# Kernel tuning notes

Measured on AMD Instinct MI355X. Metric: run time of the kernel, lower is better.

## Reference

```python
import jax, jax.numpy as jnp
import numpy as np

# Dims derived from Config for the 'ffn' pool
L, S, SE, D, K, B = 7, 200, 240, 32, 3, 512


def setup_inputs() -> dict:
    key = jax.random.key(0)
    k1, k2, k3, k4 = jax.random.split(key, 4)
    x = jax.random.normal(k1, (L, B, D), dtype=jnp.float32)
    vec_clusters = jax.random.normal(k2, (L, S, D), dtype=jnp.float32) * 0.02
    vec = jax.random.normal(k3, (L, S, SE, D), dtype=jnp.float32) * 0.02
    gain_factors = jnp.ones((L, S, SE, 2), dtype=jnp.float32)
    block_indices = jax.random.randint(k4, (L, S, SE, 2), 0, 600).astype(jnp.int32)
    return {
        'x': x,
        'vec_clusters': vec_clusters,
        'vec': vec,
        'gain_factors': gain_factors,
        'block_indices': block_indices,
    }


def reference(x, vec_clusters, vec, gain_factors, block_indices):
    # Router: score each token's query against cluster centroids. [L,B,S]
    logits = jnp.einsum('lbd,lsd->lbs', x, vec_clusters)
    top_vals, top_idx = jax.lax.top_k(logits, K)            # [L,B,K]
    probs = jax.nn.softmax(top_vals, axis=-1)               # [L,B,K]

    # Per-layer gather of the selected clusters' capacity slots.
    gather = jax.vmap(lambda tbl, idx: tbl[idx])            # map over L
    g_vec = gather(vec, top_idx)                            # [L,B,K,SE,D]
    g_gain = gather(gain_factors[..., 0], top_idx)          # [L,B,K,SE]
    g_blk = gather(block_indices[..., 0], top_idx)          # [L,B,K,SE]

    # Empty capacity slots have block index 0 (randint started at 1 in init).
    w = jax.nn.sigmoid(g_gain) * (g_blk != 0).astype(g_gain.dtype)  # [L,B,K,SE]

    # Compose parameter vectors within each selected cluster, then mix top-k.
    comp = jnp.einsum('lbke,lbked->lbkd', w, g_vec)         # [L,B,K,D]
    out = jnp.einsum('lbk,lbkd->lbd', probs, comp)          # [L,B,D]
    return out
```

## Files before the change

### kernel.cpp

```cpp
#include <hip/hip_runtime.h>
#include <math.h>

namespace {
constexpr int L = 7, S = 200, SE = 240, D = 32, B = 512;
constexpr int NTOK = L * B;
constexpr int NCLUST = L * S;
constexpr int GRID1 = NCLUST + NTOK;

template <int CTRL>
__device__ __forceinline__ float dppf(float x) {
  return __int_as_float(__builtin_amdgcn_update_dpp(
      0, __float_as_int(x), CTRL, 0xF, 0xF, true));
}
template <int CTRL>
__device__ __forceinline__ int dppi(int x) {
  return __builtin_amdgcn_update_dpp(0, x, CTRL, 0xF, 0xF, true);
}
__device__ __forceinline__ float swz16f(float x) {
  return __int_as_float(__builtin_amdgcn_ds_swizzle(__float_as_int(x), 0x401F));
}
__device__ __forceinline__ int swz16i(int x) {
  return __builtin_amdgcn_ds_swizzle(x, 0x401F);
}

__global__ __launch_bounds__(64) void fused1_kernel(
    const float* __restrict__ x,
    const float* __restrict__ vc,
    const float* __restrict__ vec,
    const float* __restrict__ gain,
    const int* __restrict__ blk,
    float* __restrict__ C,
    int4* __restrict__ tki,
    float4* __restrict__ tkp)
{
  const int lane = threadIdx.x;
  const int q = lane & 7;
  const int r8 = lane >> 3;

  if (blockIdx.x < NCLUST) {
    const int ls = blockIdx.x;
    __shared__ float sw[SE];
    for (int e = lane; e < SE; e += 64) {
      const float2 g2 = reinterpret_cast<const float2*>(gain)[ls * SE + e];
      const int2 b2 = reinterpret_cast<const int2*>(blk)[ls * SE + e];
      sw[e] = (b2.x != 0) ? 1.0f / (1.0f + __expf(-g2.x)) : 0.0f;
    }
    __syncthreads();
    const float4* v4 = reinterpret_cast<const float4*>(vec) + (size_t)ls * SE * 8;
    float4 acc = make_float4(0.f, 0.f, 0.f, 0.f);
#pragma unroll 10
    for (int k = 0; k < 30; ++k) {
      const int e = k * 8 + r8;
      const float we = sw[e];
      const float4 v = v4[e * 8 + q];
      acc.x += we * v.x; acc.y += we * v.y; acc.z += we * v.z; acc.w += we * v.w;
    }
    acc.x += dppf<0x128>(acc.x); acc.y += dppf<0x128>(acc.y);
    acc.z += dppf<0x128>(acc.z); acc.w += dppf<0x128>(acc.w);
    acc.x += swz16f(acc.x); acc.y += swz16f(acc.y);
    acc.z += swz16f(acc.z); acc.w += swz16f(acc.w);
    acc.x += __shfl_xor(acc.x, 32); acc.y += __shfl_xor(acc.y, 32);
    acc.z += __shfl_xor(acc.z, 32); acc.w += __shfl_xor(acc.w, 32);
    if (r8 == 0) reinterpret_cast<float4*>(C + ls * D)[q] = acc;
  } else {
    const int tok = blockIdx.x - NCLUST;
    const int l = tok >> 9;

    const float4 xq = reinterpret_cast<const float4*>(x + tok * D)[q];
    const float* vcl = vc + l * S * D;

    float v0 = -INFINITY, v1 = -INFINITY, v2 = -INFINITY;
    int i0 = 0x7fffffff, i1 = 0x7fffffff, i2 = 0x7fffffff;
    for (int s0 = 0; s0 < S; s0 += 8) {
      const int row = s0 + r8;
      const float4 v = reinterpret_cast<const float4*>(vcl + row * D)[q];
      float part = v.x * xq.x + v.y * xq.y + v.z * xq.z + v.w * xq.w;
      part += dppf<0xB1>(part);
      part += dppf<0x4E>(part);
      part += dppf<0x141>(part);
      if (part > v0) { v2 = v1; i2 = i1; v1 = v0; i1 = i0; v0 = part; i0 = row; }
      else if (part > v1) { v2 = v1; i2 = i1; v1 = part; i1 = row; }
      else if (part > v2) { v2 = part; i2 = row; }
    }
#pragma unroll
    for (int step = 0; step < 3; ++step) {
      float u0, u1, u2; int j0, j1, j2;
      if (step == 0) {
        u0 = dppf<0x128>(v0); u1 = dppf<0x128>(v1); u2 = dppf<0x128>(v2);
        j0 = dppi<0x128>(i0); j1 = dppi<0x128>(i1); j2 = dppi<0x128>(i2);
      } else if (step == 1) {
        u0 = swz16f(v0); u1 = swz16f(v1); u2 = swz16f(v2);
        j0 = swz16i(i0); j1 = swz16i(i1); j2 = swz16i(i2);
      } else {
        u0 = __shfl_xor(v0, 32); u1 = __shfl_xor(v1, 32); u2 = __shfl_xor(v2, 32);
        j0 = __shfl_xor(i0, 32); j1 = __shfl_xor(i1, 32); j2 = __shfl_xor(i2, 32);
      }
#pragma unroll
      for (int t = 0; t < 3; ++t) {
        const float u = (t == 0) ? u0 : (t == 1) ? u1 : u2;
        const int j = (t == 0) ? j0 : (t == 1) ? j1 : j2;
        const bool b0 = (u > v0) || (u == v0 && j < i0);
        const bool b1 = (u > v1) || (u == v1 && j < i1);
        const bool b2 = (u > v2) || (u == v2 && j < i2);
        if (b0) { v2 = v1; i2 = i1; v1 = v0; i1 = i0; v0 = u; i0 = j; }
        else if (b1) { v2 = v1; i2 = i1; v1 = u; i1 = j; }
        else if (b2) { v2 = u; i2 = j; }
      }
    }
    if (lane == 0) {
      const float e1 = __expf(v1 - v0);
      const float e2 = __expf(v2 - v0);
      const float inv = 1.f / (1.f + e1 + e2);
      tki[tok] = make_int4(i0, i1, i2, 0);
      tkp[tok] = make_float4(inv, e1 * inv, e2 * inv, 0.f);
    }
  }
}

__global__ __launch_bounds__(256) void gather_kernel(
    const float* __restrict__ C,
    const int4* __restrict__ tki,
    const float4* __restrict__ tkp,
    float* __restrict__ out)
{
  const int gid = blockIdx.x * 256 + threadIdx.x;
  const int tok = gid >> 5;
  const int d = gid & 31;
  const int l = tok >> 9;
  const int4 id = tki[tok];
  const float4 p = tkp[tok];
  const float* Cl = C + l * S * D;
  out[gid] = p.x * Cl[id.x * D + d] + p.y * Cl[id.y * D + d] + p.z * Cl[id.z * D + d];
}

}

extern "C" void kernel_launch(void* const* d_in, const int* in_sizes, int n_in,
                              void* d_out, int out_size, void* d_ws, size_t ws_size,
                              hipStream_t stream) {
  const float* x = (const float*)d_in[0];
  const float* vc = (const float*)d_in[1];
  const float* vec = (const float*)d_in[2];
  const float* gain = (const float*)d_in[3];
  const int* blk = (const int*)d_in[4];
  float* out = (float*)d_out;

  char* ws = (char*)d_ws;
  float* C = (float*)ws;
  int4* tki = (int4*)(ws + 179200);
  float4* tkp = (float4*)(ws + 179200 + 57344);

  fused1_kernel<<<GRID1, 64, 0, stream>>>(x, vc, vec, gain, blk, C, tki, tkp);
  gather_kernel<<<NTOK * D / 256, 256, 0, stream>>>(C, tki, tkp, out);
}
```

Baseline: 26.53 us.

## Make the fused router/compose kernel persistent with per-wave task loop

Replaces the launch of one 64-thread block per cluster or token with a fixed grid of 256 blocks of 8 waves. Each wave strides over a combined list of cluster-compose and token-routing tasks. Each wave gets its own shared-memory weight buffer, so the block-wide barrier is gone. This is meant to cut block scheduling overhead, but it caps residency at 8 waves per CU, which may hide memory latency less well and can leave waves unevenly loaded.

```diff
diff --git a/kernel.cpp b/kernel.cpp
--- a/kernel.cpp
+++ b/kernel.cpp
@@ -5,7 +5,10 @@
 constexpr int L = 7, S = 200, SE = 240, D = 32, B = 512;
 constexpr int NTOK = L * B;
 constexpr int NCLUST = L * S;
-constexpr int GRID1 = NCLUST + NTOK;
+constexpr int GRID1 = 256;
+constexpr int WPB = 8;
+constexpr int NWAVE = GRID1 * WPB;
+constexpr int NTASK = NCLUST + NTOK;
 
 template <int CTRL>
 __device__ __forceinline__ float dppf(float x) {
@@ -23,7 +26,7 @@
   return __builtin_amdgcn_ds_swizzle(x, 0x401F);
 }
 
-__global__ __launch_bounds__(64) void fused1_kernel(
+__global__ __launch_bounds__(512) void fused1_kernel(
     const float* __restrict__ x,
     const float* __restrict__ vc,
     const float* __restrict__ vec,
@@ -33,86 +36,90 @@
     int4* __restrict__ tki,
     float4* __restrict__ tkp)
 {
-  const int lane = threadIdx.x;
+  const int wave = threadIdx.x >> 6;
+  const int lane = threadIdx.x & 63;
+  const int W = blockIdx.x * WPB + wave;
   const int q = lane & 7;
   const int r8 = lane >> 3;
 
-  if (blockIdx.x < NCLUST) {
-    const int ls = blockIdx.x;
-    __shared__ float sw[SE];
-    for (int e = lane; e < SE; e += 64) {
-      const float2 g2 = reinterpret_cast<const float2*>(gain)[ls * SE + e];
-      const int2 b2 = reinterpret_cast<const int2*>(blk)[ls * SE + e];
-      sw[e] = (b2.x != 0) ? 1.0f / (1.0f + __expf(-g2.x)) : 0.0f;
-    }
-    __syncthreads();
-    const float4* v4 = reinterpret_cast<const float4*>(vec) + (size_t)ls * SE * 8;
-    float4 acc = make_float4(0.f, 0.f, 0.f, 0.f);
+  __shared__ float sw[WPB][SE];
+
+  for (int t = W; t < NTASK; t += NWAVE) {
+    if (t < NCLUST) {
+      const int ls = t;
+      for (int e = lane; e < SE; e += 64) {
+        const float2 g2 = reinterpret_cast<const float2*>(gain)[ls * SE + e];
+        const int2 b2 = reinterpret_cast<const int2*>(blk)[ls * SE + e];
+        sw[wave][e] = (b2.x != 0) ? 1.0f / (1.0f + __expf(-g2.x)) : 0.0f;
+      }
+      const float4* v4 = reinterpret_cast<const float4*>(vec) + (size_t)ls * SE * 8;
+      float4 acc = make_float4(0.f, 0.f, 0.f, 0.f);
 #pragma unroll 10
-    for (int k = 0; k < 30; ++k) {
-      const int e = k * 8 + r8;
-      const float we = sw[e];
-      const float4 v = v4[e * 8 + q];
-      acc.x += we * v.x; acc.y += we * v.y; acc.z += we * v.z; acc.w += we * v.w;
-    }
-    acc.x += dppf<0x128>(acc.x); acc.y += dppf<0x128>(acc.y);
-    acc.z += dppf<0x128>(acc.z); acc.w += dppf<0x128>(acc.w);
-    acc.x += swz16f(acc.x); acc.y += swz16f(acc.y);
-    acc.z += swz16f(acc.z); acc.w += swz16f(acc.w);
-    acc.x += __shfl_xor(acc.x, 32); acc.y += __shfl_xor(acc.y, 32);
-    acc.z += __shfl_xor(acc.z, 32); acc.w += __shfl_xor(acc.w, 32);
-    if (r8 == 0) reinterpret_cast<float4*>(C + ls * D)[q] = acc;
-  } else {
-    const int tok = blockIdx.x - NCLUST;
-    const int l = tok >> 9;
+      for (int k = 0; k < 30; ++k) {
+        const int e = k * 8 + r8;
+        const float we = sw[wave][e];
+        const float4 v = v4[e * 8 + q];
+        acc.x += we * v.x; acc.y += we * v.y; acc.z += we * v.z; acc.w += we * v.w;
+      }
+      acc.x += dppf<0x128>(acc.x); acc.y += dppf<0x128>(acc.y);
+      acc.z += dppf<0x128>(acc.z); acc.w += dppf<0x128>(acc.w);
+      acc.x += swz16f(acc.x); acc.y += swz16f(acc.y);
+      acc.z += swz16f(acc.z); acc.w += swz16f(acc.w);
+      acc.x += __shfl_xor(acc.x, 32); acc.y += __shfl_xor(acc.y, 32);
+      acc.z += __shfl_xor(acc.z, 32); acc.w += __shfl_xor(acc.w, 32);
+      if (r8 == 0) reinterpret_cast<float4*>(C + ls * D)[q] = acc;
+    } else {
+      const int tok = t - NCLUST;
+      const int l = tok >> 9;
 
-    const float4 xq = reinterpret_cast<const float4*>(x + tok * D)[q];
-    const float* vcl = vc + l * S * D;
+      const float4 xq = reinterpret_cast<const float4*>(x + tok * D)[q];
+      const float* vcl = vc + l * S * D;
 
-    float v0 = -INFINITY, v1 = -INFINITY, v2 = -INFINITY;
-    int i0 = 0x7fffffff, i1 = 0x7fffffff, i2 = 0x7fffffff;
-    for (int s0 = 0; s0 < S; s0 += 8) {
-      const int row = s0 + r8;
-      const float4 v = reinterpret_cast<const float4*>(vcl + row * D)[q];
-      float part = v.x * xq.x + v.y * xq.y + v.z * xq.z + v.w * xq.w;
-      part += dppf<0xB1>(part);
-      part += dppf<0x4E>(part);
-      part += dppf<0x141>(part);
-      if (part > v0) { v2 = v1; i2 = i1; v1 = v0; i1 = i0; v0 = part; i0 = row; }
-      else if (part > v1) { v2 = v1; i2 = i1; v1 = part; i1 = row; }
-      else if (part > v2) { v2 = part; i2 = row; }
-    }
-#pragma unroll
-    for (int step = 0; step < 3; ++step) {
-      float u0, u1, u2; int j0, j1, j2;
-      if (step == 0) {
-        u0 = dppf<0x128>(v0); u1 = dppf<0x128>(v1); u2 = dppf<0x128>(v2);
-        j0 = dppi<0x128>(i0); j1 = dppi<0x128>(i1); j2 = dppi<0x128>(i2);
-      } else if (step == 1) {
-        u0 = swz16f(v0); u1 = swz16f(v1); u2 = swz16f(v2);
-        j0 = swz16i(i0); j1 = swz16i(i1); j2 = swz16i(i2);
-      } else {
-        u0 = __shfl_xor(v0, 32); u1 = __shfl_xor(v1, 32); u2 = __shfl_xor(v2, 32);
-        j0 = __shfl_xor(i0, 32); j1 = __shfl_xor(i1, 32); j2 = __shfl_xor(i2, 32);
+      float v0 = -INFINITY, v1 = -INFINITY, v2 = -INFINITY;
+      int i0 = 0x7fffffff, i1 = 0x7fffffff, i2 = 0x7fffffff;
+      for (int s0 = 0; s0 < S; s0 += 8) {
+        const int row = s0 + r8;
+        const float4 v = reinterpret_cast<const float4*>(vcl + row * D)[q];
+        float part = v.x * xq.x + v.y * xq.y + v.z * xq.z + v.w * xq.w;
+        part += dppf<0xB1>(part);
+        part += dppf<0x4E>(part);
+        part += dppf<0x141>(part);
+        if (part > v0) { v2 = v1; i2 = i1; v1 = v0; i1 = i0; v0 = part; i0 = row; }
+        else if (part > v1) { v2 = v1; i2 = i1; v1 = part; i1 = row; }
+        else if (part > v2) { v2 = part; i2 = row; }
       }
 #pragma unroll
-      for (int t = 0; t < 3; ++t) {
-        const float u = (t == 0) ? u0 : (t == 1) ? u1 : u2;
-        const int j = (t == 0) ? j0 : (t == 1) ? j1 : j2;
-        const bool b0 = (u > v0) || (u == v0 && j < i0);
-        const bool b1 = (u > v1) || (u == v1 && j < i1);
-        const bool b2 = (u > v2) || (u == v2 && j < i2);
-        if (b0) { v2 = v1; i2 = i1; v1 = v0; i1 = i0; v0 = u; i0 = j; }
-        else if (b1) { v2 = v1; i2 = i1; v1 = u; i1 = j; }
-        else if (b2) { v2 = u; i2 = j; }
+      for (int step = 0; step < 3; ++step) {
+        float u0, u1, u2; int j0, j1, j2;
+        if (step == 0) {
+          u0 = dppf<0x128>(v0); u1 = dppf<0x128>(v1); u2 = dppf<0x128>(v2);
+          j0 = dppi<0x128>(i0); j1 = dppi<0x128>(i1); j2 = dppi<0x128>(i2);
+        } else if (step == 1) {
+          u0 = swz16f(v0); u1 = swz16f(v1); u2 = swz16f(v2);
+          j0 = swz16i(i0); j1 = swz16i(i1); j2 = swz16i(i2);
+        } else {
+          u0 = __shfl_xor(v0, 32); u1 = __shfl_xor(v1, 32); u2 = __shfl_xor(v2, 32);
+          j0 = __shfl_xor(i0, 32); j1 = __shfl_xor(i1, 32); j2 = __shfl_xor(i2, 32);
+        }
+#pragma unroll
+        for (int tt = 0; tt < 3; ++tt) {
+          const float u = (tt == 0) ? u0 : (tt == 1) ? u1 : u2;
+          const int j = (tt == 0) ? j0 : (tt == 1) ? j1 : j2;
+          const bool b0 = (u > v0) || (u == v0 && j < i0);
+          const bool b1 = (u > v1) || (u == v1 && j < i1);
+          const bool b2 = (u > v2) || (u == v2 && j < i2);
+          if (b0) { v2 = v1; i2 = i1; v1 = v0; i1 = i0; v0 = u; i0 = j; }
+          else if (b1) { v2 = v1; i2 = i1; v1 = u; i1 = j; }
+          else if (b2) { v2 = u; i2 = j; }
+        }
       }
-    }
-    if (lane == 0) {
-      const float e1 = __expf(v1 - v0);
-      const float e2 = __expf(v2 - v0);
-      const float inv = 1.f / (1.f + e1 + e2);
-      tki[tok] = make_int4(i0, i1, i2, 0);
-      tkp[tok] = make_float4(inv, e1 * inv, e2 * inv, 0.f);
+      if (lane == 0) {
+        const float e1 = __expf(v1 - v0);
+        const float e2 = __expf(v2 - v0);
+        const float inv = 1.f / (1.f + e1 + e2);
+        tki[tok] = make_int4(i0, i1, i2, 0);
+        tkp[tok] = make_float4(inv, e1 * inv, e2 * inv, 0.f);
+      }
     }
   }
 }
@@ -150,6 +157,6 @@
   int4* tki = (int4*)(ws + 179200);
   float4* tkp = (float4*)(ws + 179200 + 57344);
 
-  fused1_kernel<<<GRID1, 64, 0, stream>>>(x, vc, vec, gain, blk, C, tki, tkp);
+  fused1_kernel<<<GRID1, 512, 0, stream>>>(x, vc, vec, gain, blk, C, tki, tkp);
   gather_kernel<<<NTOK * D / 256, 256, 0, stream>>>(C, tki, tkp, out);
 }
```

Result: slower. 41.83 us (+57.7%).
